# Kernel tuning notes

Hardware: AMD Instinct MI355X
Metric: run time of the kernel (lower is better)

Reference implementation:

```python
import jax, jax.numpy as jnp
import numpy as np

N_VERTS = 40962  # icosphere level-6 vertex count
K_RING = 19      # 2-ring filter size


def setup_inputs() -> dict:
    key = jax.random.key(0)
    k1, k2, k3, k4 = jax.random.split(key, 4)
    B, C_in, C_out = 4, 64, 64
    x = jax.random.normal(k1, (B, C_in, N_VERTS), dtype=jnp.float32)
    neigh_orders = jax.random.randint(k2, (N_VERTS, K_RING), 0, N_VERTS, dtype=jnp.int32)
    # nn.Linear(19*in_feats, out_feats): weight [C_out, 19*C_in], bias [C_out]
    fan_in = K_RING * C_in
    bound = 1.0 / np.sqrt(fan_in)
    W = jax.random.uniform(k3, (C_out, fan_in), dtype=jnp.float32, minval=-bound, maxval=bound)
    b = jax.random.uniform(k4, (C_out,), dtype=jnp.float32, minval=-bound, maxval=bound)
    return {"x": x, "neigh_orders": neigh_orders, "W": W, "b": b}


def reference(x, neigh_orders, W, b):
    # x: [B, C_in, N] -> [B, N, C_in]
    xt = jnp.transpose(x, (0, 2, 1))
    B, N, C = xt.shape
    # gather 19-ring neighbors: [B, N, 19, C_in]
    gathered = xt[:, neigh_orders, :]
    # im2col-style flatten: [B, N, 19*C_in]
    mat = gathered.reshape(B, N, K_RING * C)
    # Linear: mat @ W.T + b -> [B, N, C_out]
    out = jnp.einsum('bnk,ok->bno', mat, W) + b
    # back to [B, C_out, N]
    return jnp.transpose(out, (0, 2, 1))
```

## Files before the change

### kernel.cpp

```cpp
#include <hip/hip_runtime.h>
#include <hip/hip_bf16.h>


#define NV   40962
#define KR   19
#define CIN  64
#define COUT 64
#define NB   4
#define NT256 161

typedef __bf16 bf16;
typedef __bf16 bf16x8 __attribute__((ext_vector_type(8)));
typedef float  floatx4 __attribute__((ext_vector_type(4)));

#define XT_ELEMS ((size_t)NB * NV * CIN)
#define WB_OFF   ((XT_ELEMS * 2 + 255) & ~(size_t)255)
#define WS_NEED  (WB_OFF + (size_t)COUT * KR * CIN * 2)

__global__ __launch_bounds__(256) void transpose_kernel(
    const float* __restrict__ x, bf16* __restrict__ xt)
{
    __shared__ float tile[64 * 65];
    const int b  = blockIdx.y;
    const int v0 = blockIdx.x * 64;
    const int t  = threadIdx.x;

    const int vl = t & 63;
    const int c0 = t >> 6;
    const int vg = min(v0 + vl, NV - 1);
    #pragma unroll
    for (int p = 0; p < 16; ++p) {
        int c = c0 * 16 + p;
        tile[vl * 65 + c] = x[((size_t)(b * CIN + c)) * NV + vg];
    }
    __syncthreads();

    const int v = t >> 2;
    const int q = t & 3;
    if (v0 + v < NV) {
        #pragma unroll
        for (int p = 0; p < 2; ++p) {
            int chunk = q + p * 4;
            bf16x8 o;
            #pragma unroll
            for (int j = 0; j < 8; ++j)
                o[j] = (bf16)tile[v * 65 + chunk * 8 + j];
            *(bf16x8*)&xt[((size_t)(b * NV + v0 + v)) * 64 + chunk * 8] = o;
        }
    }
}

__global__ __launch_bounds__(256) void convw_kernel(
    const float* __restrict__ W, bf16* __restrict__ Wf)
{
    const int idx = blockIdx.x * 256 + threadIdx.x;
    if (idx >= KR * 8 * 64) return;
    const int lane = idx & 63;
    const int f    = (idx >> 6) & 7;
    const int ring = idx >> 9;
    const int ot   = f >> 1;
    const int kc   = f & 1;
    const int row  = ot * 16 + (lane & 15);
    const int col0 = ring * 64 + kc * 32 + (lane >> 4) * 8;
    const float* src = W + (size_t)row * (KR * CIN) + col0;
    float4 a = *(const float4*)(src);
    float4 c = *(const float4*)(src + 4);
    bf16x8 o;
    o[0] = (bf16)a.x; o[1] = (bf16)a.y; o[2] = (bf16)a.z; o[3] = (bf16)a.w;
    o[4] = (bf16)c.x; o[5] = (bf16)c.y; o[6] = (bf16)c.z; o[7] = (bf16)c.w;
    *(bf16x8*)(Wf + (size_t)idx * 8) = o;
}

__global__ __launch_bounds__(256, 2) void conv_kernel(
    const int*   __restrict__ neigh,
    const bf16*  __restrict__ xt,
    const bf16*  __restrict__ Wf,
    const float* __restrict__ bias,
    float*       __restrict__ out)
{
    const int i    = blockIdx.x;
    const int b    = (i & 7) >> 1;
    const int tile = (i >> 3) * 2 + (i & 1);
    if (tile >= NT256) return;

    const int t    = threadIdx.x;
    const int wv   = t >> 6;
    const int lane = t & 63;
    const int l15  = lane & 15;
    const int g    = lane >> 4;

    const int n0 = tile * 256 + wv * 64;

    int nn[4], ib[4];
    #pragma unroll
    for (int s = 0; s < 4; ++s) {
        nn[s] = n0 + s * 16 + l15;
        ib[s] = min(nn[s], NV - 1) * KR;
    }

    const bf16* xb = xt + (((size_t)b * NV) << 6) + g * 8;
    const bf16* wb = Wf + lane * 8;

    floatx4 acc[4][4];
    #pragma unroll
    for (int s = 0; s < 4; ++s)
        #pragma unroll
        for (int o = 0; o < 4; ++o)
            acc[s][o] = (floatx4){0.f, 0.f, 0.f, 0.f};

    bf16x8 xf[4][2];
    bf16x8 wf[8];

    #pragma unroll
    for (int s = 0; s < 4; ++s) {
        int v = neigh[ib[s]];
        v = ((unsigned)v < (unsigned)NV) ? v : 0;
        const bf16* p = xb + ((size_t)v << 6);
        xf[s][0] = *(const bf16x8*)(p);
        xf[s][1] = *(const bf16x8*)(p + 32);
    }
    #pragma unroll
    for (int f = 0; f < 8; ++f)
        wf[f] = *(const bf16x8*)(wb + f * 512);

    #pragma unroll
    for (int r = 0; r < KR; ++r) {
        bf16x8 xg[4][2], wg[8];
        if (r + 1 < KR) {
            #pragma unroll
            for (int s = 0; s < 4; ++s) {
                int v = neigh[ib[s] + r + 1];
                v = ((unsigned)v < (unsigned)NV) ? v : 0;
                const bf16* p = xb + ((size_t)v << 6);
                xg[s][0] = *(const bf16x8*)(p);
                xg[s][1] = *(const bf16x8*)(p + 32);
            }
            const bf16* wr = wb + (size_t)(r + 1) * (8 * 512);
            #pragma unroll
            for (int f = 0; f < 8; ++f)
                wg[f] = *(const bf16x8*)(wr + f * 512);
        }

        #pragma unroll
        for (int kc = 0; kc < 2; ++kc)
            #pragma unroll
            for (int ot = 0; ot < 4; ++ot)
                #pragma unroll
                for (int s = 0; s < 4; ++s)
                    acc[s][ot] = __builtin_amdgcn_mfma_f32_16x16x32_bf16(
                        wf[ot * 2 + kc], xf[s][kc], acc[s][ot], 0, 0, 0);

        if (r + 1 < KR) {
            #pragma unroll
            for (int s = 0; s < 4; ++s) {
                xf[s][0] = xg[s][0];
                xf[s][1] = xg[s][1];
            }
            #pragma unroll
            for (int f = 0; f < 8; ++f)
                wf[f] = wg[f];
        }
    }

    #pragma unroll
    for (int ot = 0; ot < 4; ++ot) {
        #pragma unroll
        for (int ii = 0; ii < 4; ++ii) {
            const int o = ot * 16 + g * 4 + ii;
            const float bv = bias[o];
            #pragma unroll
            for (int s = 0; s < 4; ++s) {
                if (nn[s] < NV) {
                    out[((size_t)(b * COUT + o)) * NV + nn[s]] =
                        acc[s][ot][ii] + bv;
                }
            }
        }
    }
}

__global__ __launch_bounds__(64) void fallback_kernel(
    const int*   __restrict__ neigh,
    const float* __restrict__ x,
    const float* __restrict__ W,
    const float* __restrict__ bias,
    float*       __restrict__ out)
{
    __shared__ float xg[KR * CIN];
    const int bn = blockIdx.x;
    const int b  = bn / NV;
    const int n  = bn % NV;
    const int t  = threadIdx.x;

    for (int k = t; k < KR * CIN; k += 64) {
        int r = k / CIN, c = k - r * CIN;
        int v = neigh[n * KR + r];
        v = ((unsigned)v < (unsigned)NV) ? v : 0;
        xg[k] = x[((size_t)(b * CIN + c)) * NV + v];
    }
    __syncthreads();

    float s = bias[t];
    const float* wrow = W + (size_t)t * (KR * CIN);
    for (int k = 0; k < KR * CIN; ++k) s += xg[k] * wrow[k];
    out[((size_t)(b * COUT + t)) * NV + n] = s;
}

extern "C" void kernel_launch(void* const* d_in, const int* in_sizes, int n_in,
                              void* d_out, int out_size, void* d_ws, size_t ws_size,
                              hipStream_t stream)
{
    const float* x     = (const float*)d_in[0];
    const int*   neigh = (const int*)d_in[1];
    const float* W     = (const float*)d_in[2];
    const float* bias  = (const float*)d_in[3];
    float* out = (float*)d_out;

    if (d_ws != nullptr && ws_size >= WS_NEED) {
        bf16* xt = (bf16*)d_ws;
        bf16* Wf = (bf16*)((char*)d_ws + WB_OFF);

        dim3 tgrid((NV + 63) / 64, NB);
        transpose_kernel<<<tgrid, 256, 0, stream>>>(x, xt);
        convw_kernel<<<(KR * 8 * 64 + 255) / 256, 256, 0, stream>>>(W, Wf);

        int nblk = 8 * ((NT256 + 1) / 2);
        conv_kernel<<<nblk, 256, 0, stream>>>(neigh, xt, Wf, bias, out);
    } else {
        fallback_kernel<<<NB * NV, 64, 0, stream>>>(neigh, x, W, bias, out);
    }
}
```

Before: 185.2 us.

## Halve conv tile per block, deepen gather prefetch, load weights just-in-time

The conv kernel now processes 128 vertices per block (32 per wave) instead of 256, halving the accumulator and fragment register footprint so launch bounds can request 4 blocks per SM. The neighbor-index load is now prefetched three rings ahead and the gathered rows two rings ahead, which deepens the pipeline that hides gather latency. Weight fragments are loaded from global/L2 inside each k-chunk instead of being double-buffered in registers. The smaller tile means each weight fragment is reused across fewer vertices, so weight traffic from cache roughly doubles in exchange for higher occupancy.

New measurement: 189.6 us. 1.02x slower.

```diff
diff --git a/kernel.cpp b/kernel.cpp
--- a/kernel.cpp
+++ b/kernel.cpp
@@ -7,7 +7,7 @@
 #define CIN  64
 #define COUT 64
 #define NB   4
-#define NT256 161
+#define NTILES 321
 
 typedef __bf16 bf16;
 typedef __bf16 bf16x8 __attribute__((ext_vector_type(8)));
@@ -71,7 +71,7 @@
     *(bf16x8*)(Wf + (size_t)idx * 8) = o;
 }
 
-__global__ __launch_bounds__(256, 2) void conv_kernel(
+__global__ __launch_bounds__(256, 4) void conv_kernel(
     const int*   __restrict__ neigh,
     const bf16*  __restrict__ xt,
     const bf16*  __restrict__ Wf,
@@ -81,7 +81,7 @@
     const int i    = blockIdx.x;
     const int b    = (i & 7) >> 1;
     const int tile = (i >> 3) * 2 + (i & 1);
-    if (tile >= NT256) return;
+    if (tile >= NTILES) return;
 
     const int t    = threadIdx.x;
     const int wv   = t >> 6;
@@ -89,11 +89,11 @@
     const int l15  = lane & 15;
     const int g    = lane >> 4;
 
-    const int n0 = tile * 256 + wv * 64;
-
-    int nn[4], ib[4];
-    #pragma unroll
-    for (int s = 0; s < 4; ++s) {
+    const int n0 = tile * 128 + wv * 32;
+
+    int nn[2], ib[2];
+    #pragma unroll
+    for (int s = 0; s < 2; ++s) {
         nn[s] = n0 + s * 16 + l15;
         ib[s] = min(nn[s], NV - 1) * KR;
     }
@@ -101,64 +101,85 @@
     const bf16* xb = xt + (((size_t)b * NV) << 6) + g * 8;
     const bf16* wb = Wf + lane * 8;
 
-    floatx4 acc[4][4];
-    #pragma unroll
-    for (int s = 0; s < 4; ++s)
+    floatx4 acc[2][4];
+    #pragma unroll
+    for (int s = 0; s < 2; ++s)
         #pragma unroll
         for (int o = 0; o < 4; ++o)
             acc[s][o] = (floatx4){0.f, 0.f, 0.f, 0.f};
 
-    bf16x8 xf[4][2];
-    bf16x8 wf[8];
-
-    #pragma unroll
-    for (int s = 0; s < 4; ++s) {
-        int v = neigh[ib[s]];
-        v = ((unsigned)v < (unsigned)NV) ? v : 0;
+    int i0[2], i1[2], vic[2];
+    #pragma unroll
+    for (int s = 0; s < 2; ++s) {
+        i0[s]  = neigh[ib[s] + 0];
+        i1[s]  = neigh[ib[s] + 1];
+        vic[s] = neigh[ib[s] + 2];
+    }
+    bf16x8 xf[2][2], xg[2][2];
+    #pragma unroll
+    for (int s = 0; s < 2; ++s) {
+        int v = ((unsigned)i0[s] < (unsigned)NV) ? i0[s] : 0;
         const bf16* p = xb + ((size_t)v << 6);
         xf[s][0] = *(const bf16x8*)(p);
         xf[s][1] = *(const bf16x8*)(p + 32);
-    }
-    #pragma unroll
-    for (int f = 0; f < 8; ++f)
-        wf[f] = *(const bf16x8*)(wb + f * 512);
+        v = ((unsigned)i1[s] < (unsigned)NV) ? i1[s] : 0;
+        p = xb + ((size_t)v << 6);
+        xg[s][0] = *(const bf16x8*)(p);
+        xg[s][1] = *(const bf16x8*)(p + 32);
+    }
 
     #pragma unroll
     for (int r = 0; r < KR; ++r) {
-        bf16x8 xg[4][2], wg[8];
-        if (r + 1 < KR) {
-            #pragma unroll
-            for (int s = 0; s < 4; ++s) {
-                int v = neigh[ib[s] + r + 1];
-                v = ((unsigned)v < (unsigned)NV) ? v : 0;
+        int vid[2];
+        if (r + 3 < KR) {
+            #pragma unroll
+            for (int s = 0; s < 2; ++s)
+                vid[s] = neigh[ib[s] + r + 3];
+        }
+        bf16x8 xh[2][2];
+        if (r + 2 < KR) {
+            #pragma unroll
+            for (int s = 0; s < 2; ++s) {
+                int v = ((unsigned)vic[s] < (unsigned)NV) ? vic[s] : 0;
                 const bf16* p = xb + ((size_t)v << 6);
-                xg[s][0] = *(const bf16x8*)(p);
-                xg[s][1] = *(const bf16x8*)(p + 32);
-            }
-            const bf16* wr = wb + (size_t)(r + 1) * (8 * 512);
-            #pragma unroll
-            for (int f = 0; f < 8; ++f)
-                wg[f] = *(const bf16x8*)(wr + f * 512);
-        }
-
-        #pragma unroll
-        for (int kc = 0; kc < 2; ++kc)
+                xh[s][0] = *(const bf16x8*)(p);
+                xh[s][1] = *(const bf16x8*)(p + 32);
+            }
+        }
+
+        const bf16* wr = wb + (size_t)r * 4096;
+        #pragma unroll
+        for (int kc = 0; kc < 2; ++kc) {
+            bf16x8 wf[4];
+            #pragma unroll
+            for (int ot = 0; ot < 4; ++ot)
+                wf[ot] = *(const bf16x8*)(wr + (ot * 2 + kc) * 512);
             #pragma unroll
             for (int ot = 0; ot < 4; ++ot)
                 #pragma unroll
-                for (int s = 0; s < 4; ++s)
+                for (int s = 0; s < 2; ++s)
                     acc[s][ot] = __builtin_amdgcn_mfma_f32_16x16x32_bf16(
-                        wf[ot * 2 + kc], xf[s][kc], acc[s][ot], 0, 0, 0);
+                        wf[ot], xf[s][kc], acc[s][ot], 0, 0, 0);
+        }
 
         if (r + 1 < KR) {
             #pragma unroll
-            for (int s = 0; s < 4; ++s) {
+            for (int s = 0; s < 2; ++s) {
                 xf[s][0] = xg[s][0];
                 xf[s][1] = xg[s][1];
             }
-            #pragma unroll
-            for (int f = 0; f < 8; ++f)
-                wf[f] = wg[f];
+        }
+        if (r + 2 < KR) {
+            #pragma unroll
+            for (int s = 0; s < 2; ++s) {
+                xg[s][0] = xh[s][0];
+                xg[s][1] = xh[s][1];
+            }
+        }
+        if (r + 3 < KR) {
+            #pragma unroll
+            for (int s = 0; s < 2; ++s)
+                vic[s] = vid[s];
         }
     }
 
@@ -169,7 +190,7 @@
             const int o = ot * 16 + g * 4 + ii;
             const float bv = bias[o];
             #pragma unroll
-            for (int s = 0; s < 4; ++s) {
+            for (int s = 0; s < 2; ++s) {
                 if (nn[s] < NV) {
                     out[((size_t)(b * COUT + o)) * NV + nn[s]] =
                         acc[s][ot][ii] + bv;
@@ -224,7 +245,7 @@
         transpose_kernel<<<tgrid, 256, 0, stream>>>(x, xt);
         convw_kernel<<<(KR * 8 * 64 + 255) / 256, 256, 0, stream>>>(W, Wf);
 
-        int nblk = 8 * ((NT256 + 1) / 2);
+        int nblk = 8 * ((NTILES + 1) / 2);
         conv_kernel<<<nblk, 256, 0, stream>>>(neigh, xt, Wf, bias, out);
     } else {
         fallback_kernel<<<NB * NV, 64, 0, stream>>>(neigh, x, W, bias, out);
```
